# Kernel tuning notes

Hardware: AMD Instinct MI355X
Metric: run time of the kernel (lower is better)

## Reference

```python
import jax, jax.numpy as jnp
import numpy as np

N, B, D = 50000, 128, 35   # nodes, graphs, node_dim
T = 140                     # padded sequence length
EPS = 1e-5

def _gcn(x, W, b, src, dst):
    # PyG GCNConv: sym-normalized adjacency with self loops, then linear.
    h = x @ W
    deg = jnp.ones((N,), h.dtype).at[dst].add(1.0)  # in-degree + self loop
    dinv = jax.lax.rsqrt(deg)
    msg = h[src] * (dinv[src] * dinv[dst])[:, None]
    agg = jax.ops.segment_sum(msg, dst, num_segments=N)
    return agg + h * (dinv * dinv)[:, None] + b  # + self-loop messages + bias

def _bn(x, g, b):
    m = x.mean(0)
    v = x.var(0)
    return (x - m) * jax.lax.rsqrt(v + EPS) * g + b

def _lstm(xs, Wih, Whh, bih, bhh, reverse):
    # xs: [T, B, D]; torch LSTM gate order i,f,g,o; hidden size D
    def step(carry, xt):
        h, c = carry
        gates = xt @ Wih.T + h @ Whh.T + bih + bhh
        i, f, g, o = jnp.split(gates, 4, axis=-1)
        c = jax.nn.sigmoid(f) * c + jax.nn.sigmoid(i) * jnp.tanh(g)
        h = jax.nn.sigmoid(o) * jnp.tanh(c)
        return (h, c), h
    h0 = jnp.zeros((xs.shape[1], D), xs.dtype)
    _, hs = jax.lax.scan(step, (h0, h0), xs, reverse=reverse)
    return hs

def setup_inputs() -> dict:
    key = jax.random.key(0)
    ks = iter(jax.random.split(key, 64))
    def w(shape, s=0.05):
        return jax.random.normal(next(ks), shape, jnp.float32) * s
    inp = {
        'x': jax.random.normal(next(ks), (N, D), jnp.float32),
        'edge_intra': jax.random.randint(next(ks), (2, 300000), 0, N, jnp.int32),
        'edge_inter': jax.random.randint(next(ks), (2, 100000), 0, N, jnp.int32),
        'split': jax.random.randint(next(ks), (N,), 0, 2, jnp.int32),
        'batch': jnp.sort(jax.random.randint(next(ks), (N,), 0, B, jnp.int32)),
    }
    dims = [(35, 128), (128, 256), (256, 512), (512, 256), (256, 35)]
    for i, (di, do) in enumerate(dims, 1):
        inp[f'W{i}'] = w((di, do)); inp[f'b{i}'] = jnp.zeros((do,), jnp.float32)
        inp[f'g{i}'] = jnp.ones((do,), jnp.float32); inp[f'be{i}'] = jnp.zeros((do,), jnp.float32)
    for d in ('f', 'b'):  # bidirectional LSTM, 4*D = 140 gate rows
        inp[f'Wih_{d}'] = w((4 * D, D)); inp[f'Whh_{d}'] = w((4 * D, D))
        inp[f'bih_{d}'] = jnp.zeros((4 * D,), jnp.float32); inp[f'bhh_{d}'] = jnp.zeros((4 * D,), jnp.float32)
    for nm in ('q', 'k', 'v'):  # attention over d=2*D=70
        inp[f'W{nm}'] = w((2 * D, 2 * D)); inp[f'b{nm}'] = jnp.zeros((2 * D,), jnp.float32)
    inp['Wfc1'] = w((9800, 4340), 0.01); inp['bfc1'] = jnp.zeros((4340,), jnp.float32)
    inp['Wfc2'] = w((4340, 1), 0.01); inp['bfc2'] = jnp.zeros((1,), jnp.float32)
    return inp

def reference(x, edge_intra, edge_inter, split, batch,
              W1, b1, g1, be1, W2, b2, g2, be2, W3, b3, g3, be3,
              W4, b4, g4, be4, W5, b5, g5, be5,
              Wih_f, Whh_f, bih_f, bhh_f, Wih_b, Whh_b, bih_b, bhh_b,
              Wq, bq, Wk, bk, Wv, bv, Wfc1, bfc1, Wfc2, bfc2):
    src = jnp.concatenate([edge_intra[0], edge_inter[0]])
    dst = jnp.concatenate([edge_intra[1], edge_inter[1]])
    # conv1-3: relu then bn; conv4: bn then relu; conv5: bn only
    h = _bn(jax.nn.relu(_gcn(x, W1, b1, src, dst)), g1, be1)
    h = _bn(jax.nn.relu(_gcn(h, W2, b2, src, dst)), g2, be2)
    h = _bn(jax.nn.relu(_gcn(h, W3, b3, src, dst)), g3, be3)
    h = jax.nn.relu(_bn(_gcn(h, W4, b4, src, dst), g4, be4))
    h = _bn(_gcn(h, W5, b5, src, dst), g5, be5)
    # masked global_add_pool per split (avoids dynamic boolean indexing)
    is_pro = (split == 1).astype(h.dtype)[:, None]
    pro = jax.ops.segment_sum(h * is_pro, batch, num_segments=B)
    lig = jax.ops.segment_sum(h * (1.0 - is_pro), batch, num_segments=B)
    seq = jnp.concatenate([lig, pro], axis=1).reshape(B, 2, D)  # L = 2
    seq = jnp.pad(seq, ((0, 0), (0, T - 2), (0, 0)))            # [B,140,35]
    # attention mask, L=2 (static)
    m = jnp.eye(T, dtype=jnp.float32)
    m = m.at[2:, :].set(0.0).at[:, 2:].set(0.0)
    m = m.at[:, 1].set(1.0).at[1, :].set(1.0).at[1, 1].set(0.0)
    # BiLSTM over time axis
    xs = seq.transpose(1, 0, 2)  # [T,B,35]
    hf = _lstm(xs, Wih_f, Whh_f, bih_f, bhh_f, False)
    hb = _lstm(xs, Wih_b, Whh_b, bih_b, bhh_b, True)
    out = jnp.concatenate([hf, hb], axis=-1).transpose(1, 0, 2)  # [B,140,70]
    # masked single-head attention
    q = out @ Wq + bq
    k = out @ Wk + bk
    v = out @ Wv + bv
    sc = jnp.einsum('bqd,bkd->bqk', q, k) / jnp.sqrt(jnp.asarray(2.0 * D, out.dtype))
    sc = jnp.where(m[None] == 0, -1e9, sc)
    o = jax.nn.softmax(sc, axis=-1) @ v  # [B,140,70]
    f = jax.nn.relu(o.reshape(B, -1) @ Wfc1 + bfc1)
    return (f @ Wfc2 + bfc2).reshape(-1)
```

## Files before the change

### kernel.cpp

```cpp
#include <hip/hip_runtime.h>

#define N_NODES 50000
#define DIM0 35
#define BGRAPH 128
#define TSEQ 140
#define EPSBN 1e-5f
#define E_TOTAL 400000
#define E_INTRA 300000
#define E_INTER 100000
#define FC1_OUT 4340

typedef __attribute__((ext_vector_type(8))) short s8v;
typedef __attribute__((ext_vector_type(4))) short s4v;
typedef __attribute__((ext_vector_type(4))) float f32x4;

static __device__ __forceinline__ unsigned short bf16_rne(float x) {
    unsigned int u = __float_as_uint(x);
    unsigned int r = (u + 0x7FFFu + ((u >> 16) & 1u)) >> 16;
    return (unsigned short)r;
}
static __device__ __forceinline__ void bf16_split(float x, unsigned short& h, unsigned short& l) {
    h = bf16_rne(x);
    float hf = __uint_as_float(((unsigned int)h) << 16);
    l = bf16_rne(x - hf);
}

static __device__ __forceinline__ void edge_sd(int e, const int* intra, const int* inter, int& s, int& d) {
    if (e < E_INTRA) { s = intra[e]; d = intra[E_INTRA + e]; }
    else { int k = e - E_INTRA; s = inter[k]; d = inter[E_INTER + k]; }
}

__global__ void k_init(int* cnt, int* cursor, float* out, const float* bfc2, float* bnsumAll) {
    int i = blockIdx.x * 256 + threadIdx.x;
    if (i < N_NODES) { cnt[i] = 0; cursor[i] = 0; }
    if (i < BGRAPH) out[i] = bfc2[0];
    if (i < 5 * 1024) bnsumAll[i] = 0.f;
}

__global__ void k_deg(const int* intra, const int* inter, int* cnt) {
    int e = blockIdx.x * 256 + threadIdx.x;
    if (e >= E_TOTAL) return;
    int s, d; edge_sd(e, intra, inter, s, d);
    atomicAdd(&cnt[d], 1);
}

__global__ void k_scan1(const int* __restrict__ cnt, int* __restrict__ partial, int* __restrict__ blocksum,
                        float* __restrict__ dinv) {
    __shared__ int buf[256];
    int t = threadIdx.x;
    int i = blockIdx.x * 256 + t;
    int v = (i < N_NODES) ? cnt[i] : 0;
    if (i < N_NODES) dinv[i] = rsqrtf(1.0f + (float)v);
    buf[t] = v;
    __syncthreads();
    for (int off = 1; off < 256; off <<= 1) {
        int add = (t >= off) ? buf[t - off] : 0;
        __syncthreads();
        buf[t] += add;
        __syncthreads();
    }
    if (i < N_NODES) partial[i] = buf[t];
    if (t == 255) blocksum[blockIdx.x] = buf[255];
}

__global__ void k_scan2(int* blocksum, int nb) {
    __shared__ int buf[256];
    int t = threadIdx.x;
    buf[t] = (t < nb) ? blocksum[t] : 0;
    __syncthreads();
    for (int off = 1; off < 256; off <<= 1) {
        int add = (t >= off) ? buf[t - off] : 0;
        __syncthreads();
        buf[t] += add;
        __syncthreads();
    }
    if (t < nb) blocksum[t] = buf[t];
}

__global__ void k_scan3(const int* __restrict__ partial, const int* __restrict__ blocksum, int* __restrict__ rowptr) {
    int b = blockIdx.x;
    int i = b * 256 + threadIdx.x;
    if (i == 0) rowptr[0] = 0;
    if (i < N_NODES) {
        int off = (b == 0) ? 0 : blocksum[b - 1];
        rowptr[i + 1] = partial[i] + off;
    }
}

__global__ void k_scatter(const int* intra, const int* inter, const int* rowptr,
                          int* cursor, const float* dinv, int* srcs, float* coef) {
    int e = blockIdx.x * 256 + threadIdx.x;
    if (e >= E_TOTAL) return;
    int s, d; edge_sd(e, intra, inter, s, d);
    int p = rowptr[d] + atomicAdd(&cursor[d], 1);
    srcs[p] = s;
    coef[p] = dinv[s] * dinv[d];
}

__global__ __launch_bounds__(256) void k_agg_small(const float* __restrict__ X, float* __restrict__ Z,
        const int* __restrict__ rowptr, const int* __restrict__ srcs, const float* __restrict__ coef,
        const float* __restrict__ dinv, const float* __restrict__ bias) {
    int wave = threadIdx.x >> 6, lane = threadIdx.x & 63;
    int i = blockIdx.x * 4 + wave;
    if (i >= N_NODES || lane >= DIM0) return;
    int b0 = rowptr[i], e1 = rowptr[i + 1];
    float self = dinv[i] * dinv[i];
    float acc = X[(size_t)i * DIM0 + lane] * self;
    if (bias) acc += bias[lane];
    for (int k = b0; k < e1; ++k) acc += coef[k] * X[(size_t)srcs[k] * DIM0 + lane];
    Z[(size_t)i * DIM0 + lane] = acc;
}

__global__ __launch_bounds__(256) void k_agg_vec(const float* __restrict__ X, float* __restrict__ Z,
        const int* __restrict__ rowptr, const int* __restrict__ srcs, const float* __restrict__ coef,
        const float* __restrict__ dinv, const float* __restrict__ alpha, const float* __restrict__ beta,
        const float* __restrict__ bias, int d, int lpshift) {
    int i = (blockIdx.x * 256 + threadIdx.x) >> lpshift;
    int lane_in = threadIdx.x & ((1 << lpshift) - 1);
    if (i >= N_NODES) return;
    int b0 = rowptr[i], e1 = rowptr[i + 1];
    float self = dinv[i] * dinv[i];
    int c = lane_in * 4;
    float4 al, be;
    if (alpha) { al = *(const float4*)&alpha[c]; be = *(const float4*)&beta[c]; }
    else { al = make_float4(1.f, 1.f, 1.f, 1.f); be = make_float4(0.f, 0.f, 0.f, 0.f); }
    float4 xi = *(const float4*)&X[(size_t)i * d + c];
    float4 acc;
    acc.x = self * (al.x * xi.x + be.x);
    acc.y = self * (al.y * xi.y + be.y);
    acc.z = self * (al.z * xi.z + be.z);
    acc.w = self * (al.w * xi.w + be.w);
    if (bias) {
        float4 bi = *(const float4*)&bias[c];
        acc.x += bi.x; acc.y += bi.y; acc.z += bi.z; acc.w += bi.w;
    }
    for (int k = b0; k < e1; ++k) {
        int s = srcs[k];
        float cf = coef[k];
        float4 xs = *(const float4*)&X[(size_t)s * d + c];
        acc.x += cf * (al.x * xs.x + be.x);
        acc.y += cf * (al.y * xs.y + be.y);
        acc.z += cf * (al.z * xs.z + be.z);
        acc.w += cf * (al.w * xs.w + be.w);
    }
    *(float4*)&Z[(size_t)i * d + c] = acc;
}

__global__ __launch_bounds__(256) void k_gemm(const float* __restrict__ A, const float* __restrict__ W,
                                              const float* __restrict__ bias, float* __restrict__ C,
                                              int Mrows, int K, int Ncols, int relu,
                                              const float* __restrict__ alphaA, const float* __restrict__ betaA,
                                              int reluA) {
    __shared__ float As[64][17];
    __shared__ float Ws[16][65];
    int tid = threadIdx.x;
    int tx = tid & 15, ty = tid >> 4;
    int row0 = blockIdx.x * 64, col0 = blockIdx.y * 64;
    float acc[4][4] = {};
    for (int k0 = 0; k0 < K; k0 += 16) {
        for (int l = tid; l < 1024; l += 256) {
            int m = l >> 4, kk = l & 15;
            int r = row0 + m, k = k0 + kk;
            float v = 0.f;
            if (r < Mrows && k < K) {
                v = A[(size_t)r * K + k];
                if (alphaA) {
                    v = alphaA[k] * v + betaA[k];
                    if (reluA) v = fmaxf(v, 0.f);
                }
            }
            As[m][kk] = v;
        }
        for (int l = tid; l < 1024; l += 256) {
            int kk = l >> 6, n = l & 63;
            int k = k0 + kk, c = col0 + n;
            Ws[kk][n] = (k < K && c < Ncols) ? W[(size_t)k * Ncols + c] : 0.f;
        }
        __syncthreads();
#pragma unroll
        for (int kk = 0; kk < 16; ++kk) {
            float a[4], w[4];
#pragma unroll
            for (int i2 = 0; i2 < 4; ++i2) a[i2] = As[ty * 4 + i2][kk];
#pragma unroll
            for (int j = 0; j < 4; ++j) w[j] = Ws[kk][tx * 4 + j];
#pragma unroll
            for (int i2 = 0; i2 < 4; ++i2)
#pragma unroll
                for (int j = 0; j < 4; ++j)
                    acc[i2][j] += a[i2] * w[j];
        }
        __syncthreads();
    }
    for (int i2 = 0; i2 < 4; ++i2) {
        int r = row0 + ty * 4 + i2;
        if (r >= Mrows) continue;
        for (int j = 0; j < 4; ++j) {
            int c = col0 + tx * 4 + j;
            if (c >= Ncols) continue;
            float v = acc[i2][j];
            if (bias) v += bias[c];
            if (relu) v = fmaxf(v, 0.f);
            C[(size_t)r * Ncols + c] = v;
        }
    }
}

__global__ void k_wprep(const float* __restrict__ W, unsigned short* __restrict__ Wf, int K, int Ncols) {
    int gid = blockIdx.x * 256 + threadIdx.x;
    int KT = K >> 5;
    int total = (Ncols >> 4) * KT * 64;
    if (gid >= total) return;
    int lane = gid & 63;
    int f = gid >> 6;
    int kt = f % KT, ntile = f / KT;
    int n = ntile * 16 + (lane & 15);
    int kb = kt * 32 + (lane >> 4) * 8;
    size_t base = (size_t)f * 1024 + lane * 8;
#pragma unroll
    for (int j = 0; j < 8; ++j) {
        unsigned short h, l;
        bf16_split(W[(size_t)(kb + j) * Ncols + n], h, l);
        Wf[base + j] = h;
        Wf[base + 512 + j] = l;
    }
}

__global__ __launch_bounds__(256) void k_gemm_mfma(
    const float* __restrict__ A, const unsigned short* __restrict__ Wf,
    const float* __restrict__ bias, float* __restrict__ C,
    int Mrows, int K, int Ncols, int relu,
    const float* __restrict__ alphaA, const float* __restrict__ betaA,
    float* __restrict__ bnsum) {
    __shared__ unsigned short As[2][2][128][40];
    int tid = threadIdx.x;
    int lane = tid & 63, wave = tid >> 6;
    int wm = wave >> 1, wn = wave & 1;
    int row0 = blockIdx.x * 128;
    int nt0 = blockIdx.y * 8;
    int KT = K >> 5;

    f32x4 acc[4][4];
#pragma unroll
    for (int a = 0; a < 4; ++a)
#pragma unroll
        for (int b = 0; b < 4; ++b) acc[a][b] = (f32x4)0.f;

    float4 reg[4];
    auto load_chunk = [&](int kt) {
#pragma unroll
        for (int l = 0; l < 4; ++l) {
            int i = tid + l * 256;
            int m = i >> 3, kv = (i & 7) * 4;
            int r = row0 + m;
            float4 v = make_float4(0.f, 0.f, 0.f, 0.f);
            if (r < Mrows) v = *(const float4*)&A[(size_t)r * K + kt * 32 + kv];
            reg[l] = v;
        }
    };
    auto store_chunk = [&](int buf, int kt) {
#pragma unroll
        for (int l = 0; l < 4; ++l) {
            int i = tid + l * 256;
            int m = i >> 3, kv = (i & 7) * 4;
            float4 v = reg[l];
            if (alphaA) {
                int kg = kt * 32 + kv;
                float4 al = *(const float4*)&alphaA[kg];
                float4 be = *(const float4*)&betaA[kg];
                v.x = al.x * v.x + be.x;
                v.y = al.y * v.y + be.y;
                v.z = al.z * v.z + be.z;
                v.w = al.w * v.w + be.w;
            }
            unsigned short h0, l0, h1, l1, h2, l2, h3, l3;
            bf16_split(v.x, h0, l0); bf16_split(v.y, h1, l1);
            bf16_split(v.z, h2, l2); bf16_split(v.w, h3, l3);
            s4v hv = {(short)h0, (short)h1, (short)h2, (short)h3};
            s4v lv = {(short)l0, (short)l1, (short)l2, (short)l3};
            *(s4v*)&As[buf][0][m][kv] = hv;
            *(s4v*)&As[buf][1][m][kv] = lv;
        }
    };

    load_chunk(0);
    store_chunk(0, 0);
    __syncthreads();

    int mrow = wm * 64 + (lane & 15);
    int koff = (lane >> 4) * 8;

    for (int kt = 0; kt < KT; ++kt) {
        int cur = kt & 1;
        if (kt + 1 < KT) load_chunk(kt + 1);
        s8v bh[4], bl[4];
#pragma unroll
        for (int nt = 0; nt < 4; ++nt) {
            int ntg = nt0 + wn * 4 + nt;
            size_t fb = ((size_t)(ntg * KT + kt)) * 1024 + lane * 8;
            bh[nt] = *(const s8v*)&Wf[fb];
            bl[nt] = *(const s8v*)&Wf[fb + 512];
        }
        s8v ah[4], alo[4];
#pragma unroll
        for (int mt = 0; mt < 4; ++mt) {
            ah[mt]  = *(const s8v*)&As[cur][0][mrow + mt * 16][koff];
            alo[mt] = *(const s8v*)&As[cur][1][mrow + mt * 16][koff];
        }
#pragma unroll
        for (int nt = 0; nt < 4; ++nt)
#pragma unroll
            for (int mt = 0; mt < 4; ++mt) {
                acc[mt][nt] = __builtin_amdgcn_mfma_f32_16x16x32_bf16(ah[mt], bh[nt], acc[mt][nt], 0, 0, 0);
                acc[mt][nt] = __builtin_amdgcn_mfma_f32_16x16x32_bf16(ah[mt], bl[nt], acc[mt][nt], 0, 0, 0);
                acc[mt][nt] = __builtin_amdgcn_mfma_f32_16x16x32_bf16(alo[mt], bh[nt], acc[mt][nt], 0, 0, 0);
            }
        if (kt + 1 < KT) store_chunk(cur ^ 1, kt + 1);
        __syncthreads();
    }

#pragma unroll
    for (int nt = 0; nt < 4; ++nt) {
        int cg = (nt0 + wn * 4 + nt) * 16 + (lane & 15);
        float bia = bias ? bias[cg] : 0.f;
        float s1 = 0.f, s2 = 0.f;
#pragma unroll
        for (int mt = 0; mt < 4; ++mt) {
            int rbase = row0 + wm * 64 + mt * 16 + (lane >> 4) * 4;
#pragma unroll
            for (int r = 0; r < 4; ++r) {
                int rg = rbase + r;
                if (rg < Mrows) {
                    float v = acc[mt][nt][r] + bia;
                    if (relu) v = fmaxf(v, 0.f);
                    C[(size_t)rg * Ncols + cg] = v;
                    s1 += v; s2 += v * v;
                }
            }
        }
        if (bnsum) {
            s1 += __shfl_xor(s1, 16, 64);
            s1 += __shfl_xor(s1, 32, 64);
            s2 += __shfl_xor(s2, 16, 64);
            s2 += __shfl_xor(s2, 32, 64);
            if (lane < 16) {
                atomicAdd(&bnsum[cg], s1);
                atomicAdd(&bnsum[Ncols + cg], s2);
            }
        }
    }
}

__global__ void k_bn_stats(const float* __restrict__ X, float* sums, int d) {
    long long total = (long long)N_NODES * d;
    int G = gridDim.x * blockDim.x;
    int gid = blockIdx.x * blockDim.x + threadIdx.x;
    int c = gid % d;
    float s1 = 0.f, s2 = 0.f;
    for (long long i = gid; i < total; i += G) {
        float v = X[i];
        s1 += v; s2 += v * v;
    }
    atomicAdd(&sums[c], s1);
    atomicAdd(&sums[d + c], s2);
}

__global__ void k_bn_final(const float* sums, const float* g, const float* be,
                           float* alpha, float* beta, int d) {
    int c = threadIdx.x;
    if (c >= d) return;
    float mean = sums[c] / (float)N_NODES;
    float var = sums[d + c] / (float)N_NODES - mean * mean;
    float a = g[c] * rsqrtf(var + EPSBN);
    alpha[c] = a;
    beta[c] = be[c] - mean * a;
}

__global__ void k_pool(const float* __restrict__ h, const int* __restrict__ split,
                       const int* __restrict__ batch, float* lig, float* pro,
                       const float* __restrict__ alpha, const float* __restrict__ beta) {
    int b = blockIdx.x;
    __shared__ float sl[DIM0], sp[DIM0];
    __shared__ int s_start, s_end;
    if (threadIdx.x < DIM0) { sl[threadIdx.x] = 0.f; sp[threadIdx.x] = 0.f; }
    if (threadIdx.x == 0) {
        int lo = 0, hi = N_NODES;
        while (lo < hi) { int mid = (lo + hi) >> 1; if (batch[mid] < b) lo = mid + 1; else hi = mid; }
        s_start = lo;
        hi = N_NODES;
        while (lo < hi) { int mid = (lo + hi) >> 1; if (batch[mid] < b + 1) lo = mid + 1; else hi = mid; }
        s_end = lo;
    }
    __syncthreads();
    int start = s_start, end = s_end;
    for (int k = threadIdx.x; k < (end - start) * DIM0; k += blockDim.x) {
        int node = start + k / DIM0;
        int c = k % DIM0;
        float v = alpha[c] * h[(size_t)node * DIM0 + c] + beta[c];
        if (split[node] == 1) atomicAdd(&sp[c], v);
        else atomicAdd(&sl[c], v);
    }
    __syncthreads();
    if (threadIdx.x < DIM0) {
        lig[b * DIM0 + threadIdx.x] = sl[threadIdx.x];
        pro[b * DIM0 + threadIdx.x] = sp[threadIdx.x];
    }
}

__global__ __launch_bounds__(192) void k_lstm(
    const float* __restrict__ lig, const float* __restrict__ pro,
    const float* __restrict__ Wih_f, const float* __restrict__ Whh_f,
    const float* __restrict__ bih_f, const float* __restrict__ bhh_f,
    const float* __restrict__ Wih_b, const float* __restrict__ Whh_b,
    const float* __restrict__ bih_b, const float* __restrict__ bhh_b,
    float* __restrict__ outb) {
    int blk = blockIdx.x;
    int dir = blk >> 7;
    int b = blk & 127;
    const float* Wih = dir ? Wih_b : Wih_f;
    const float* Whh = dir ? Whh_b : Whh_f;
    const float* bih = dir ? bih_b : bih_f;
    const float* bhh = dir ? bhh_b : bhh_f;

    __shared__ float h_lds[DIM0];
    __shared__ float x_lds[2][DIM0];
    __shared__ float gate_lds[4 * DIM0];
    int t = threadIdx.x;
    float wih[DIM0], whh[DIM0], bsum = 0.f;
    if (t < 4 * DIM0) {
#pragma unroll
        for (int j = 0; j < DIM0; ++j) { wih[j] = Wih[t * DIM0 + j]; whh[j] = Whh[t * DIM0 + j]; }
        bsum = bih[t] + bhh[t];
    }
    if (t < DIM0) {
        x_lds[0][t] = lig[b * DIM0 + t];
        x_lds[1][t] = pro[b * DIM0 + t];
        h_lds[t] = 0.f;
    }
    float c_reg = 0.f;
    __syncthreads();
    for (int step = 0; step < TSEQ; ++step) {
        int tt = dir ? (TSEQ - 1 - step) : step;
        if (t < 4 * DIM0) {
            float acc = bsum;
            if (tt < 2) {
#pragma unroll
                for (int j = 0; j < DIM0; ++j) acc += wih[j] * x_lds[tt][j];
            }
#pragma unroll
            for (int j = 0; j < DIM0; ++j) acc += whh[j] * h_lds[j];
            gate_lds[t] = acc;
        }
        __syncthreads();
        if (t < DIM0) {
            float gi = gate_lds[t], gf = gate_lds[DIM0 + t];
            float gg = gate_lds[2 * DIM0 + t], go = gate_lds[3 * DIM0 + t];
            float si = 1.f / (1.f + expf(-gi));
            float sf = 1.f / (1.f + expf(-gf));
            float so = 1.f / (1.f + expf(-go));
            c_reg = sf * c_reg + si * tanhf(gg);
            float hv = so * tanhf(c_reg);
            h_lds[t] = hv;
            outb[((size_t)b * TSEQ + tt) * 70 + dir * DIM0 + t] = hv;
        }
        __syncthreads();
    }
}

__global__ void k_concatW(const float* __restrict__ Wq, const float* __restrict__ bq,
                          const float* __restrict__ Wk, const float* __restrict__ bk,
                          const float* __restrict__ Wv, const float* __restrict__ bv,
                          float* __restrict__ Wcat, float* __restrict__ bcat) {
    int idx = blockIdx.x * 256 + threadIdx.x;
    if (idx < 70 * 210) {
        int k = idx / 210, col = idx % 210;
        int g = col / 70, j = col % 70;
        const float* Wsrc = (g == 0) ? Wq : ((g == 1) ? Wk : Wv);
        Wcat[idx] = Wsrc[k * 70 + j];
    }
    if (idx < 210) {
        int g = idx / 70, j = idx % 70;
        const float* bsrc = (g == 0) ? bq : ((g == 1) ? bk : bv);
        bcat[idx] = bsrc[j];
    }
}

__global__ void k_attention(const float* __restrict__ qkv, float* __restrict__ osm) {
    int b = blockIdx.x;
    __shared__ float q0[70], q1[70], s[TSEQ];
    __shared__ float s00_s, s01_s, ssum_s;
    int t = threadIdx.x;
    const float* base = qkv + (size_t)b * TSEQ * 210;
    if (t < 70) {
        q0[t] = base[0 * 210 + t];
        q1[t] = base[1 * 210 + t];
    }
    __syncthreads();
    const float scale = rsqrtf(70.f);
    if (t < TSEQ) {
        const float* krow = base + (size_t)t * 210 + 70;
        float acc = 0.f;
        for (int j = 0; j < 70; ++j) acc += q1[j] * krow[j];
        s[t] = acc * scale;
    } else if (t == TSEQ || t == TSEQ + 1) {
        int kk = t - TSEQ;
        const float* krow = base + (size_t)kk * 210 + 70;
        float acc = 0.f;
        for (int j = 0; j < 70; ++j) acc += q0[j] * krow[j];
        if (kk) s01_s = acc * scale; else s00_s = acc * scale;
    }
    __syncthreads();
    if (t == 0) {
        float mx = -1e30f;
        for (int i = 0; i < TSEQ; ++i) if (i != 1) mx = fmaxf(mx, s[i]);
        float sum = 0.f;
        for (int i = 0; i < TSEQ; ++i) {
            float e = (i == 1) ? 0.f : expf(s[i] - mx);
            s[i] = e; sum += e;
        }
        ssum_s = sum;
    }
    __syncthreads();
    if (t < 70) {
        float inv = 1.f / ssum_s;
        float acc = 0.f;
        for (int i = 0; i < TSEQ; ++i) acc += s[i] * base[(size_t)i * 210 + 140 + t];
        float o1v = acc * inv;
        float m0 = fmaxf(s00_s, s01_s);
        float e0 = expf(s00_s - m0), e1 = expf(s01_s - m0);
        float w0 = e0 / (e0 + e1), w1 = e1 / (e0 + e1);
        float v0 = base[0 * 210 + 140 + t];
        float v1 = base[1 * 210 + 140 + t];
        osm[b * 210 + t] = w0 * v0 + w1 * v1;
        osm[b * 210 + 70 + t] = o1v;
        osm[b * 210 + 140 + t] = v1;
    }
}

__global__ void k_wsum(const float* __restrict__ Wfc1, float* __restrict__ Wsum) {
    int idx = blockIdx.x * 256 + threadIdx.x;
    if (idx >= 70 * FC1_OUT) return;
    int j = idx / FC1_OUT, c = idx % FC1_OUT;
    float acc = 0.f;
    for (int tt = 2; tt < TSEQ; ++tt) acc += Wfc1[((size_t)(tt * 70 + j)) * FC1_OUT + c];
    Wsum[(size_t)j * FC1_OUT + c] = acc;
}

__global__ __launch_bounds__(256) void k_fc(const float* __restrict__ osm, const float* __restrict__ Wfc1,
                                            const float* __restrict__ Wsum, const float* __restrict__ bfc1,
                                            const float* __restrict__ Wfc2, float* __restrict__ out) {
    __shared__ float olds[8][210];
    __shared__ float wred[4][8];
    int g = blockIdx.y;
    int c = blockIdx.x * 256 + threadIdx.x;
    for (int l = threadIdx.x; l < 8 * 210; l += 256)
        olds[l / 210][l % 210] = osm[(g * 8 + l / 210) * 210 + (l % 210)];
    __syncthreads();
    float acc[8] = {};
    if (c < FC1_OUT) {
        for (int j = 0; j < 140; ++j) {
            float w = Wfc1[(size_t)j * FC1_OUT + c];
#pragma unroll
            for (int b = 0; b < 8; ++b) acc[b] = fmaf(olds[b][j], w, acc[b]);
        }
        for (int j = 0; j < 70; ++j) {
            float w = Wsum[(size_t)j * FC1_OUT + c];
#pragma unroll
            for (int b = 0; b < 8; ++b) acc[b] = fmaf(olds[b][140 + j], w, acc[b]);
        }
        float bb = bfc1[c], pw = Wfc2[c];
#pragma unroll
        for (int b = 0; b < 8; ++b) acc[b] = fmaxf(acc[b] + bb, 0.f) * pw;
    }
#pragma unroll
    for (int b = 0; b < 8; ++b) {
        acc[b] += __shfl_down(acc[b], 32, 64);
        acc[b] += __shfl_down(acc[b], 16, 64);
        acc[b] += __shfl_down(acc[b], 8, 64);
        acc[b] += __shfl_down(acc[b], 4, 64);
        acc[b] += __shfl_down(acc[b], 2, 64);
        acc[b] += __shfl_down(acc[b], 1, 64);
    }
    int wave = threadIdx.x >> 6;
    if ((threadIdx.x & 63) == 0)
#pragma unroll
        for (int b = 0; b < 8; ++b) wred[wave][b] = acc[b];
    __syncthreads();
    if (threadIdx.x < 8) {
        float t = wred[0][threadIdx.x] + wred[1][threadIdx.x] + wred[2][threadIdx.x] + wred[3][threadIdx.x];
        atomicAdd(&out[g * 8 + threadIdx.x], t);
    }
}

extern "C" void kernel_launch(void* const* d_in, const int* in_sizes, int n_in,
                              void* d_out, int out_size, void* d_ws, size_t ws_size,
                              hipStream_t stream) {
    const float* x = (const float*)d_in[0];
    const int* intra = (const int*)d_in[1];
    const int* inter = (const int*)d_in[2];
    const int* split = (const int*)d_in[3];
    const int* batch = (const int*)d_in[4];
    const float *W[5], *bW[5], *gW[5], *beW[5];
    for (int i = 0; i < 5; ++i) {
        W[i]   = (const float*)d_in[5 + 4 * i];
        bW[i]  = (const float*)d_in[6 + 4 * i];
        gW[i]  = (const float*)d_in[7 + 4 * i];
        beW[i] = (const float*)d_in[8 + 4 * i];
    }
    const float* Wih_f = (const float*)d_in[25];
    const float* Whh_f = (const float*)d_in[26];
    const float* bih_f = (const float*)d_in[27];
    const float* bhh_f = (const float*)d_in[28];
    const float* Wih_b = (const float*)d_in[29];
    const float* Whh_b = (const float*)d_in[30];
    const float* bih_b = (const float*)d_in[31];
    const float* bhh_b = (const float*)d_in[32];
    const float* Wq = (const float*)d_in[33];
    const float* bq = (const float*)d_in[34];
    const float* Wk = (const float*)d_in[35];
    const float* bk = (const float*)d_in[36];
    const float* Wv = (const float*)d_in[37];
    const float* bv = (const float*)d_in[38];
    const float* Wfc1 = (const float*)d_in[39];
    const float* bfc1 = (const float*)d_in[40];
    const float* Wfc2 = (const float*)d_in[41];
    const float* bfc2 = (const float*)d_in[42];

    char* p = (char*)d_ws;
    auto carve = [&](size_t bytes) {
        char* r = p;
        p += (bytes + 255) & ~(size_t)255;
        return r;
    };
    float* bufA = (float*)carve((size_t)N_NODES * 512 * 4);
    float* bufB = (float*)carve((size_t)N_NODES * 256 * 4);
    float* bufM = (float*)carve((size_t)N_NODES * 256 * 4);
    float* dinv = (float*)carve((size_t)N_NODES * 4);
    int* cnt    = (int*)carve((size_t)N_NODES * 4);
    int* rowptr = (int*)carve((size_t)(N_NODES + 1) * 4);
    int* cursor = (int*)carve((size_t)N_NODES * 4);
    int* scanp  = (int*)carve((size_t)N_NODES * 4);
    int* bsums  = (int*)carve(256 * 4);
    int* srcs   = (int*)carve((size_t)E_TOTAL * 4);
    float* coef = (float*)carve((size_t)E_TOTAL * 4);
    float* bnsumAll = (float*)carve(5 * 1024 * 4);
    float* alphaAll = (float*)carve(5 * 512 * 4);
    float* betaAll  = (float*)carve(5 * 512 * 4);
    float* lig = (float*)carve((size_t)BGRAPH * DIM0 * 4);
    float* pro = (float*)carve((size_t)BGRAPH * DIM0 * 4);
    float* outb = (float*)carve((size_t)BGRAPH * TSEQ * 70 * 4);
    float* qkvb = (float*)carve((size_t)BGRAPH * TSEQ * 210 * 4);
    float* Wcat = (float*)carve((size_t)70 * 210 * 4);
    float* bcat = (float*)carve(210 * 4);
    float* osm = (float*)carve((size_t)BGRAPH * 210 * 4);
    float* wsum = (float*)carve((size_t)70 * FC1_OUT * 4);
    unsigned short* Wf2 = (unsigned short*)carve((size_t)128 * 256 * 2 * 2);
    unsigned short* Wf3 = (unsigned short*)carve((size_t)256 * 512 * 2 * 2);
    unsigned short* Wf4 = (unsigned short*)carve((size_t)512 * 256 * 2 * 2);

    float* out = (float*)d_out;

    const int SCAN_B = (N_NODES + 255) / 256;

    k_init<<<(N_NODES + 255) / 256, 256, 0, stream>>>(cnt, cursor, out, bfc2, bnsumAll);
    k_deg<<<(E_TOTAL + 255) / 256, 256, 0, stream>>>(intra, inter, cnt);
    k_scan1<<<SCAN_B, 256, 0, stream>>>(cnt, scanp, bsums, dinv);
    k_scan2<<<1, 256, 0, stream>>>(bsums, SCAN_B);
    k_scan3<<<SCAN_B, 256, 0, stream>>>(scanp, bsums, rowptr);
    k_scatter<<<(E_TOTAL + 255) / 256, 256, 0, stream>>>(intra, inter, rowptr, cursor, dinv, srcs, coef);
    k_concatW<<<(70 * 210 + 255) / 256, 256, 0, stream>>>(Wq, bq, Wk, bk, Wv, bv, Wcat, bcat);
    k_wprep<<<((256 / 16) * (128 / 32) * 64 + 255) / 256, 256, 0, stream>>>(W[1], Wf2, 128, 256);
    k_wprep<<<((512 / 16) * (256 / 32) * 64 + 255) / 256, 256, 0, stream>>>(W[2], Wf3, 256, 512);
    k_wprep<<<((256 / 16) * (512 / 32) * 64 + 255) / 256, 256, 0, stream>>>(W[3], Wf4, 512, 256);

    auto BN = [&](int layer) { return bnsumAll + layer * 1024; };
    auto AL = [&](int layer) { return alphaAll + layer * 512; };
    auto BE = [&](int layer) { return betaAll + layer * 512; };
    auto bn_final = [&](int layer, int d) {
        k_bn_final<<<1, 512, 0, stream>>>(BN(layer), gW[layer], beW[layer], AL(layer), BE(layer), d);
    };

    const int GB64 = (N_NODES + 63) / 64;
    const int GB128 = (N_NODES + 127) / 128;
    const int AGG4 = (N_NODES + 3) / 4;
    const int AGG8 = (N_NODES + 7) / 8;

    k_agg_small<<<AGG4, 256, 0, stream>>>(x, bufM, rowptr, srcs, coef, dinv, nullptr);
    k_gemm<<<dim3(GB64, 2), 256, 0, stream>>>(bufM, W[0], bW[0], bufA, N_NODES, 35, 128, 1, nullptr, nullptr, 0);
    k_bn_stats<<<128, 256, 0, stream>>>(bufA, BN(0), 128);
    bn_final(0, 128);
    k_agg_vec<<<AGG8, 256, 0, stream>>>(bufA, bufM, rowptr, srcs, coef, dinv, AL(0), BE(0), nullptr, 128, 5);
    k_gemm_mfma<<<dim3(GB128, 2), 256, 0, stream>>>(bufM, Wf2, bW[1], bufB, N_NODES, 128, 256, 1, nullptr, nullptr, BN(1));
    bn_final(1, 256);
    k_agg_vec<<<AGG4, 256, 0, stream>>>(bufB, bufM, rowptr, srcs, coef, dinv, AL(1), BE(1), nullptr, 256, 6);
    k_gemm_mfma<<<dim3(GB128, 4), 256, 0, stream>>>(bufM, Wf3, bW[2], bufA, N_NODES, 256, 512, 1, nullptr, nullptr, BN(2));
    bn_final(2, 512);
    k_gemm_mfma<<<dim3(GB128, 2), 256, 0, stream>>>(bufA, Wf4, nullptr, bufM, N_NODES, 512, 256, 0, AL(2), BE(2), nullptr);
    k_agg_vec<<<AGG4, 256, 0, stream>>>(bufM, bufB, rowptr, srcs, coef, dinv, nullptr, nullptr, bW[3], 256, 6);
    k_bn_stats<<<256, 256, 0, stream>>>(bufB, BN(3), 256);
    bn_final(3, 256);
    k_gemm<<<dim3(GB64, 1), 256, 0, stream>>>(bufB, W[4], nullptr, bufM, N_NODES, 256, 35, 0, AL(3), BE(3), 1);
    k_agg_small<<<AGG4, 256, 0, stream>>>(bufM, bufA, rowptr, srcs, coef, dinv, bW[4]);
    k_bn_stats<<<35, 256, 0, stream>>>(bufA, BN(4), 35);
    bn_final(4, 35);

    k_pool<<<BGRAPH, 256, 0, stream>>>(bufA, split, batch, lig, pro, AL(4), BE(4));

    k_lstm<<<256, 192, 0, stream>>>(lig, pro, Wih_f, Whh_f, bih_f, bhh_f,
                                    Wih_b, Whh_b, bih_b, bhh_b, outb);

    k_gemm<<<dim3((BGRAPH * TSEQ + 63) / 64, 4), 256, 0, stream>>>(outb, Wcat, bcat, qkvb,
                                                                   BGRAPH * TSEQ, 70, 210, 0, nullptr, nullptr, 0);

    k_attention<<<BGRAPH, 256, 0, stream>>>(qkvb, osm);

    k_wsum<<<(70 * FC1_OUT + 255) / 256, 256, 0, stream>>>(Wfc1, wsum);
    k_fc<<<dim3(17, 16), 256, 0, stream>>>(osm, Wfc1, wsum, bfc1, Wfc2, out);
}
```

Measured before the change: 1.087 ms.

## Pre-split GEMM activations into bf16 hi/lo in producers and fold BN into weights

The aggregation and GEMM epilogues now write activations directly as separate bf16 hi and lo arrays, so the MFMA GEMM loads bf16 tiles straight into LDS and no longer converts fp32 per tile. For layer 4 the BatchNorm affine is folded into the weight prep (row scale) plus a precomputed bias vector instead of being applied to activations. Buffers are reorganized and aliased. This cuts the fp32 A-operand traffic and the per-block split work, at the cost of the layer-3 GEMM writing two bf16 outputs and a small serial bias kernel.

Result: slower. 1.198 ms (+10.2%).

```diff
diff --git a/kernel.cpp b/kernel.cpp
--- a/kernel.cpp
+++ b/kernel.cpp
@@ -113,27 +113,48 @@
 
 __global__ __launch_bounds__(256) void k_agg_vec(const float* __restrict__ X, float* __restrict__ Z,
         const int* __restrict__ rowptr, const int* __restrict__ srcs, const float* __restrict__ coef,
-        const float* __restrict__ dinv, const float* __restrict__ alpha, const float* __restrict__ beta,
-        const float* __restrict__ bias, int d, int lpshift) {
+        const float* __restrict__ dinv, const float* __restrict__ bias, int d, int lpshift) {
     int i = (blockIdx.x * 256 + threadIdx.x) >> lpshift;
     int lane_in = threadIdx.x & ((1 << lpshift) - 1);
     if (i >= N_NODES) return;
     int b0 = rowptr[i], e1 = rowptr[i + 1];
     float self = dinv[i] * dinv[i];
     int c = lane_in * 4;
-    float4 al, be;
-    if (alpha) { al = *(const float4*)&alpha[c]; be = *(const float4*)&beta[c]; }
-    else { al = make_float4(1.f, 1.f, 1.f, 1.f); be = make_float4(0.f, 0.f, 0.f, 0.f); }
+    float4 xi = *(const float4*)&X[(size_t)i * d + c];
+    float4 acc;
+    acc.x = self * xi.x; acc.y = self * xi.y; acc.z = self * xi.z; acc.w = self * xi.w;
+    if (bias) {
+        float4 bi = *(const float4*)&bias[c];
+        acc.x += bi.x; acc.y += bi.y; acc.z += bi.z; acc.w += bi.w;
+    }
+    for (int k = b0; k < e1; ++k) {
+        int s = srcs[k];
+        float cf = coef[k];
+        float4 xs = *(const float4*)&X[(size_t)s * d + c];
+        acc.x += cf * xs.x; acc.y += cf * xs.y; acc.z += cf * xs.z; acc.w += cf * xs.w;
+    }
+    *(float4*)&Z[(size_t)i * d + c] = acc;
+}
+
+__global__ __launch_bounds__(256) void k_agg_split(const float* __restrict__ X,
+        unsigned short* __restrict__ Ahi, unsigned short* __restrict__ Alo,
+        const int* __restrict__ rowptr, const int* __restrict__ srcs, const float* __restrict__ coef,
+        const float* __restrict__ dinv, const float* __restrict__ alpha, const float* __restrict__ beta,
+        int d, int lpshift) {
+    int i = (blockIdx.x * 256 + threadIdx.x) >> lpshift;
+    int lane_in = threadIdx.x & ((1 << lpshift) - 1);
+    if (i >= N_NODES) return;
+    int b0 = rowptr[i], e1 = rowptr[i + 1];
+    float self = dinv[i] * dinv[i];
+    int c = lane_in * 4;
+    float4 al = *(const float4*)&alpha[c];
+    float4 be = *(const float4*)&beta[c];
     float4 xi = *(const float4*)&X[(size_t)i * d + c];
     float4 acc;
     acc.x = self * (al.x * xi.x + be.x);
     acc.y = self * (al.y * xi.y + be.y);
     acc.z = self * (al.z * xi.z + be.z);
     acc.w = self * (al.w * xi.w + be.w);
-    if (bias) {
-        float4 bi = *(const float4*)&bias[c];
-        acc.x += bi.x; acc.y += bi.y; acc.z += bi.z; acc.w += bi.w;
-    }
     for (int k = b0; k < e1; ++k) {
         int s = srcs[k];
         float cf = coef[k];
@@ -143,7 +164,13 @@
         acc.z += cf * (al.z * xs.z + be.z);
         acc.w += cf * (al.w * xs.w + be.w);
     }
-    *(float4*)&Z[(size_t)i * d + c] = acc;
+    unsigned short h0, l0, h1, l1, h2, l2, h3, l3;
+    bf16_split(acc.x, h0, l0); bf16_split(acc.y, h1, l1);
+    bf16_split(acc.z, h2, l2); bf16_split(acc.w, h3, l3);
+    s4v hv = {(short)h0, (short)h1, (short)h2, (short)h3};
+    s4v lv = {(short)l0, (short)l1, (short)l2, (short)l3};
+    *(s4v*)&Ahi[(size_t)i * d + c] = hv;
+    *(s4v*)&Alo[(size_t)i * d + c] = lv;
 }
 
 __global__ __launch_bounds__(256) void k_gemm(const float* __restrict__ A, const float* __restrict__ W,
@@ -206,7 +233,8 @@
     }
 }
 
-__global__ void k_wprep(const float* __restrict__ W, unsigned short* __restrict__ Wf, int K, int Ncols) {
+__global__ void k_wprep(const float* __restrict__ W, unsigned short* __restrict__ Wf, int K, int Ncols,
+                        const float* __restrict__ rowscale) {
     int gid = blockIdx.x * 256 + threadIdx.x;
     int KT = K >> 5;
     int total = (Ncols >> 4) * KT * 64;
@@ -219,19 +247,29 @@
     size_t base = (size_t)f * 1024 + lane * 8;
 #pragma unroll
     for (int j = 0; j < 8; ++j) {
+        float v = W[(size_t)(kb + j) * Ncols + n];
+        if (rowscale) v *= rowscale[kb + j];
         unsigned short h, l;
-        bf16_split(W[(size_t)(kb + j) * Ncols + n], h, l);
+        bf16_split(v, h, l);
         Wf[base + j] = h;
         Wf[base + 512 + j] = l;
     }
 }
 
-__global__ __launch_bounds__(256) void k_gemm_mfma(
-    const float* __restrict__ A, const unsigned short* __restrict__ Wf,
-    const float* __restrict__ bias, float* __restrict__ C,
-    int Mrows, int K, int Ncols, int relu,
-    const float* __restrict__ alphaA, const float* __restrict__ betaA,
-    float* __restrict__ bnsum) {
+__global__ void k_bnbias(const float* __restrict__ W, const float* __restrict__ beta,
+                         float* __restrict__ bv, int K, int Ncols) {
+    int c = blockIdx.x * 256 + threadIdx.x;
+    if (c >= Ncols) return;
+    float acc = 0.f;
+    for (int k = 0; k < K; ++k) acc += beta[k] * W[(size_t)k * Ncols + c];
+    bv[c] = acc;
+}
+
+__global__ __launch_bounds__(256) void k_gemm_mfma2(
+    const unsigned short* __restrict__ Ahi, const unsigned short* __restrict__ Alo,
+    const unsigned short* __restrict__ Wf, const float* __restrict__ bias,
+    float* __restrict__ C, unsigned short* __restrict__ Chi, unsigned short* __restrict__ Clo,
+    int Mrows, int K, int Ncols, int relu, float* __restrict__ bnsum) {
     __shared__ unsigned short As[2][2][128][40];
     int tid = threadIdx.x;
     int lane = tid & 63, wave = tid >> 6;
@@ -246,53 +284,42 @@
 #pragma unroll
         for (int b = 0; b < 4; ++b) acc[a][b] = (f32x4)0.f;
 
-    float4 reg[4];
-    auto load_chunk = [&](int kt) {
-#pragma unroll
-        for (int l = 0; l < 4; ++l) {
-            int i = tid + l * 256;
-            int m = i >> 3, kv = (i & 7) * 4;
+    s8v rh[2], rl[2];
+    auto stage_regs = [&](int kt) {
+#pragma unroll
+        for (int l = 0; l < 2; ++l) {
+            int j = tid + l * 256;
+            int m = j >> 2, ko = (j & 3) * 8;
             int r = row0 + m;
-            float4 v = make_float4(0.f, 0.f, 0.f, 0.f);
-            if (r < Mrows) v = *(const float4*)&A[(size_t)r * K + kt * 32 + kv];
-            reg[l] = v;
+            s8v h = (s8v)0, lo = (s8v)0;
+            if (r < Mrows) {
+                size_t off = (size_t)r * K + kt * 32 + ko;
+                h = *(const s8v*)&Ahi[off];
+                lo = *(const s8v*)&Alo[off];
+            }
+            rh[l] = h; rl[l] = lo;
         }
     };
-    auto store_chunk = [&](int buf, int kt) {
-#pragma unroll
-        for (int l = 0; l < 4; ++l) {
-            int i = tid + l * 256;
-            int m = i >> 3, kv = (i & 7) * 4;
-            float4 v = reg[l];
-            if (alphaA) {
-                int kg = kt * 32 + kv;
-                float4 al = *(const float4*)&alphaA[kg];
-                float4 be = *(const float4*)&betaA[kg];
-                v.x = al.x * v.x + be.x;
-                v.y = al.y * v.y + be.y;
-                v.z = al.z * v.z + be.z;
-                v.w = al.w * v.w + be.w;
-            }
-            unsigned short h0, l0, h1, l1, h2, l2, h3, l3;
-            bf16_split(v.x, h0, l0); bf16_split(v.y, h1, l1);
-            bf16_split(v.z, h2, l2); bf16_split(v.w, h3, l3);
-            s4v hv = {(short)h0, (short)h1, (short)h2, (short)h3};
-            s4v lv = {(short)l0, (short)l1, (short)l2, (short)l3};
-            *(s4v*)&As[buf][0][m][kv] = hv;
-            *(s4v*)&As[buf][1][m][kv] = lv;
+    auto write_lds = [&](int buf) {
+#pragma unroll
+        for (int l = 0; l < 2; ++l) {
+            int j = tid + l * 256;
+            int m = j >> 2, ko = (j & 3) * 8;
+            *(s8v*)&As[buf][0][m][ko] = rh[l];
+            *(s8v*)&As[buf][1][m][ko] = rl[l];
         }
     };
 
-    load_chunk(0);
-    store_chunk(0, 0);
+    stage_regs(0);
+    write_lds(0);
     __syncthreads();
 
     int mrow = wm * 64 + (lane & 15);
     int koff = (lane >> 4) * 8;
+    int cur = 0;
 
     for (int kt = 0; kt < KT; ++kt) {
-        int cur = kt & 1;
-        if (kt + 1 < KT) load_chunk(kt + 1);
+        if (kt + 1 < KT) stage_regs(kt + 1);
         s8v bh[4], bl[4];
 #pragma unroll
         for (int nt = 0; nt < 4; ++nt) {
@@ -315,8 +342,9 @@
                 acc[mt][nt] = __builtin_amdgcn_mfma_f32_16x16x32_bf16(ah[mt], bl[nt], acc[mt][nt], 0, 0, 0);
                 acc[mt][nt] = __builtin_amdgcn_mfma_f32_16x16x32_bf16(alo[mt], bh[nt], acc[mt][nt], 0, 0, 0);
             }
-        if (kt + 1 < KT) store_chunk(cur ^ 1, kt + 1);
-        __syncthreads();
+        if (kt + 1 < KT) write_lds(cur ^ 1);
+        __syncthreads();
+        cur ^= 1;
     }
 
 #pragma unroll
@@ -333,7 +361,13 @@
                 if (rg < Mrows) {
                     float v = acc[mt][nt][r] + bia;
                     if (relu) v = fmaxf(v, 0.f);
-                    C[(size_t)rg * Ncols + cg] = v;
+                    if (C) C[(size_t)rg * Ncols + cg] = v;
+                    if (Chi) {
+                        unsigned short h, l;
+                        bf16_split(v, h, l);
+                        Chi[(size_t)rg * Ncols + cg] = h;
+                        Clo[(size_t)rg * Ncols + cg] = l;
+                    }
                     s1 += v; s2 += v * v;
                 }
             }
@@ -632,7 +666,13 @@
         p += (bytes + 255) & ~(size_t)255;
         return r;
     };
-    float* bufA = (float*)carve((size_t)N_NODES * 512 * 4);
+    unsigned short* A2hi = (unsigned short*)carve((size_t)N_NODES * 128 * 2);
+    unsigned short* A2lo = (unsigned short*)carve((size_t)N_NODES * 128 * 2);
+    unsigned short* A3hi = (unsigned short*)carve((size_t)N_NODES * 256 * 2);
+    unsigned short* A3lo = (unsigned short*)carve((size_t)N_NODES * 256 * 2);
+    unsigned short* A4hi = (unsigned short*)carve((size_t)N_NODES * 512 * 2);
+    unsigned short* A4lo = (unsigned short*)carve((size_t)N_NODES * 512 * 2);
+    float* bufA = (float*)carve((size_t)N_NODES * 128 * 4);
     float* bufB = (float*)carve((size_t)N_NODES * 256 * 4);
     float* bufM = (float*)carve((size_t)N_NODES * 256 * 4);
     float* dinv = (float*)carve((size_t)N_NODES * 4);
@@ -646,17 +686,18 @@
     float* bnsumAll = (float*)carve(5 * 1024 * 4);
     float* alphaAll = (float*)carve(5 * 512 * 4);
     float* betaAll  = (float*)carve(5 * 512 * 4);
+    float* bv4  = (float*)carve(256 * 4);
     float* lig = (float*)carve((size_t)BGRAPH * DIM0 * 4);
     float* pro = (float*)carve((size_t)BGRAPH * DIM0 * 4);
-    float* outb = (float*)carve((size_t)BGRAPH * TSEQ * 70 * 4);
-    float* qkvb = (float*)carve((size_t)BGRAPH * TSEQ * 210 * 4);
     float* Wcat = (float*)carve((size_t)70 * 210 * 4);
     float* bcat = (float*)carve(210 * 4);
     float* osm = (float*)carve((size_t)BGRAPH * 210 * 4);
-    float* wsum = (float*)carve((size_t)70 * FC1_OUT * 4);
     unsigned short* Wf2 = (unsigned short*)carve((size_t)128 * 256 * 2 * 2);
     unsigned short* Wf3 = (unsigned short*)carve((size_t)256 * 512 * 2 * 2);
     unsigned short* Wf4 = (unsigned short*)carve((size_t)512 * 256 * 2 * 2);
+    float* outb = (float*)A2hi;
+    float* qkvb = outb + (size_t)BGRAPH * TSEQ * 70;
+    float* wsum = qkvb + (size_t)BGRAPH * TSEQ * 210;
 
     float* out = (float*)d_out;
 
@@ -669,9 +710,8 @@
     k_scan3<<<SCAN_B, 256, 0, stream>>>(scanp, bsums, rowptr);
     k_scatter<<<(E_TOTAL + 255) / 256, 256, 0, stream>>>(intra, inter, rowptr, cursor, dinv, srcs, coef);
     k_concatW<<<(70 * 210 + 255) / 256, 256, 0, stream>>>(Wq, bq, Wk, bk, Wv, bv, Wcat, bcat);
-    k_wprep<<<((256 / 16) * (128 / 32) * 64 + 255) / 256, 256, 0, stream>>>(W[1], Wf2, 128, 256);
-    k_wprep<<<((512 / 16) * (256 / 32) * 64 + 255) / 256, 256, 0, stream>>>(W[2], Wf3, 256, 512);
-    k_wprep<<<((256 / 16) * (512 / 32) * 64 + 255) / 256, 256, 0, stream>>>(W[3], Wf4, 512, 256);
+    k_wprep<<<((256 / 16) * (128 / 32) * 64 + 255) / 256, 256, 0, stream>>>(W[1], Wf2, 128, 256, nullptr);
+    k_wprep<<<((512 / 16) * (256 / 32) * 64 + 255) / 256, 256, 0, stream>>>(W[2], Wf3, 256, 512, nullptr);
 
     auto BN = [&](int layer) { return bnsumAll + layer * 1024; };
     auto AL = [&](int layer) { return alphaAll + layer * 512; };
@@ -689,14 +729,19 @@
     k_gemm<<<dim3(GB64, 2), 256, 0, stream>>>(bufM, W[0], bW[0], bufA, N_NODES, 35, 128, 1, nullptr, nullptr, 0);
     k_bn_stats<<<128, 256, 0, stream>>>(bufA, BN(0), 128);
     bn_final(0, 128);
-    k_agg_vec<<<AGG8, 256, 0, stream>>>(bufA, bufM, rowptr, srcs, coef, dinv, AL(0), BE(0), nullptr, 128, 5);
-    k_gemm_mfma<<<dim3(GB128, 2), 256, 0, stream>>>(bufM, Wf2, bW[1], bufB, N_NODES, 128, 256, 1, nullptr, nullptr, BN(1));
+    k_agg_split<<<AGG8, 256, 0, stream>>>(bufA, A2hi, A2lo, rowptr, srcs, coef, dinv, AL(0), BE(0), 128, 5);
+    k_gemm_mfma2<<<dim3(GB128, 2), 256, 0, stream>>>(A2hi, A2lo, Wf2, bW[1], bufB, nullptr, nullptr,
+                                                     N_NODES, 128, 256, 1, BN(1));
     bn_final(1, 256);
-    k_agg_vec<<<AGG4, 256, 0, stream>>>(bufB, bufM, rowptr, srcs, coef, dinv, AL(1), BE(1), nullptr, 256, 6);
-    k_gemm_mfma<<<dim3(GB128, 4), 256, 0, stream>>>(bufM, Wf3, bW[2], bufA, N_NODES, 256, 512, 1, nullptr, nullptr, BN(2));
+    k_agg_split<<<AGG4, 256, 0, stream>>>(bufB, A3hi, A3lo, rowptr, srcs, coef, dinv, AL(1), BE(1), 256, 6);
+    k_gemm_mfma2<<<dim3(GB128, 4), 256, 0, stream>>>(A3hi, A3lo, Wf3, bW[2], nullptr, A4hi, A4lo,
+                                                     N_NODES, 256, 512, 1, BN(2));
     bn_final(2, 512);
-    k_gemm_mfma<<<dim3(GB128, 2), 256, 0, stream>>>(bufA, Wf4, nullptr, bufM, N_NODES, 512, 256, 0, AL(2), BE(2), nullptr);
-    k_agg_vec<<<AGG4, 256, 0, stream>>>(bufM, bufB, rowptr, srcs, coef, dinv, nullptr, nullptr, bW[3], 256, 6);
+    k_wprep<<<((256 / 16) * (512 / 32) * 64 + 255) / 256, 256, 0, stream>>>(W[3], Wf4, 512, 256, AL(2));
+    k_bnbias<<<1, 256, 0, stream>>>(W[3], BE(2), bv4, 512, 256);
+    k_gemm_mfma2<<<dim3(GB128, 2), 256, 0, stream>>>(A4hi, A4lo, Wf4, bv4, bufM, nullptr, nullptr,
+                                                     N_NODES, 512, 256, 0, nullptr);
+    k_agg_vec<<<AGG4, 256, 0, stream>>>(bufM, bufB, rowptr, srcs, coef, dinv, bW[3], 256, 6);
     k_bn_stats<<<256, 256, 0, stream>>>(bufB, BN(3), 256);
     bn_final(3, 256);
     k_gemm<<<dim3(GB64, 1), 256, 0, stream>>>(bufB, W[4], nullptr, bufM, N_NODES, 256, 35, 0, AL(3), BE(3), 1);
```

## Fold BN affine into layer-4 weights and swap grid axes for row-tile locality

Applied to the files above, without the earlier changes.

The batch-norm scale of layer 3 is folded into the bf16-split weights of the layer-4 GEMM, and its shift becomes a precomputed bias vector accumulated by a new small kernel. This removes the per-element alpha/beta transform from the GEMM's A-load path. All GEMM launches also swap grid x/y so that column tiles of the same row block run next to each other, which should improve L2 reuse of A. The cost is an extra weight-prep pass and an atomic bias kernel sitting between the layer-3 GEMM and the layer-4 GEMM. Because the weights are scaled before the bf16 split, rounding changes slightly.

Measured after the change: 1.072 ms. No clear change (-1.4%).

```diff
diff --git a/kernel.cpp b/kernel.cpp
--- a/kernel.cpp
+++ b/kernel.cpp
@@ -30,11 +30,12 @@
     else { int k = e - E_INTRA; s = inter[k]; d = inter[E_INTER + k]; }
 }
 
-__global__ void k_init(int* cnt, int* cursor, float* out, const float* bfc2, float* bnsumAll) {
+__global__ void k_init(int* cnt, int* cursor, float* out, const float* bfc2, float* bnsumAll, float* bv4) {
     int i = blockIdx.x * 256 + threadIdx.x;
     if (i < N_NODES) { cnt[i] = 0; cursor[i] = 0; }
     if (i < BGRAPH) out[i] = bfc2[0];
     if (i < 5 * 1024) bnsumAll[i] = 0.f;
+    if (i < 256) bv4[i] = 0.f;
 }
 
 __global__ void k_deg(const int* intra, const int* inter, int* cnt) {
@@ -155,7 +156,7 @@
     __shared__ float Ws[16][65];
     int tid = threadIdx.x;
     int tx = tid & 15, ty = tid >> 4;
-    int row0 = blockIdx.x * 64, col0 = blockIdx.y * 64;
+    int row0 = blockIdx.y * 64, col0 = blockIdx.x * 64;
     float acc[4][4] = {};
     for (int k0 = 0; k0 < K; k0 += 16) {
         for (int l = tid; l < 1024; l += 256) {
@@ -206,7 +207,8 @@
     }
 }
 
-__global__ void k_wprep(const float* __restrict__ W, unsigned short* __restrict__ Wf, int K, int Ncols) {
+__global__ void k_wprep(const float* __restrict__ W, unsigned short* __restrict__ Wf, int K, int Ncols,
+                        const float* __restrict__ rowscale) {
     int gid = blockIdx.x * 256 + threadIdx.x;
     int KT = K >> 5;
     int total = (Ncols >> 4) * KT * 64;
@@ -219,11 +221,24 @@
     size_t base = (size_t)f * 1024 + lane * 8;
 #pragma unroll
     for (int j = 0; j < 8; ++j) {
+        float v = W[(size_t)(kb + j) * Ncols + n];
+        if (rowscale) v *= rowscale[kb + j];
         unsigned short h, l;
-        bf16_split(W[(size_t)(kb + j) * Ncols + n], h, l);
+        bf16_split(v, h, l);
         Wf[base + j] = h;
         Wf[base + 512 + j] = l;
     }
+}
+
+__global__ void k_bnbias(const float* __restrict__ W, const float* __restrict__ beta,
+                         float* __restrict__ bv, int K, int Ncols) {
+    int c = threadIdx.x;
+    if (c >= Ncols) return;
+    int k0 = blockIdx.x * 16;
+    float acc = 0.f;
+#pragma unroll
+    for (int k = 0; k < 16; ++k) acc += beta[k0 + k] * W[(size_t)(k0 + k) * Ncols + c];
+    atomicAdd(&bv[c], acc);
 }
 
 __global__ __launch_bounds__(256) void k_gemm_mfma(
@@ -236,8 +251,8 @@
     int tid = threadIdx.x;
     int lane = tid & 63, wave = tid >> 6;
     int wm = wave >> 1, wn = wave & 1;
-    int row0 = blockIdx.x * 128;
-    int nt0 = blockIdx.y * 8;
+    int row0 = blockIdx.y * 128;
+    int nt0 = blockIdx.x * 8;
     int KT = K >> 5;
 
     f32x4 acc[4][4];
@@ -646,6 +661,7 @@
     float* bnsumAll = (float*)carve(5 * 1024 * 4);
     float* alphaAll = (float*)carve(5 * 512 * 4);
     float* betaAll  = (float*)carve(5 * 512 * 4);
+    float* bv4  = (float*)carve(256 * 4);
     float* lig = (float*)carve((size_t)BGRAPH * DIM0 * 4);
     float* pro = (float*)carve((size_t)BGRAPH * DIM0 * 4);
     float* outb = (float*)carve((size_t)BGRAPH * TSEQ * 70 * 4);
@@ -662,16 +678,15 @@
 
     const int SCAN_B = (N_NODES + 255) / 256;
 
-    k_init<<<(N_NODES + 255) / 256, 256, 0, stream>>>(cnt, cursor, out, bfc2, bnsumAll);
+    k_init<<<(N_NODES + 255) / 256, 256, 0, stream>>>(cnt, cursor, out, bfc2, bnsumAll, bv4);
     k_deg<<<(E_TOTAL + 255) / 256, 256, 0, stream>>>(intra, inter, cnt);
     k_scan1<<<SCAN_B, 256, 0, stream>>>(cnt, scanp, bsums, dinv);
     k_scan2<<<1, 256, 0, stream>>>(bsums, SCAN_B);
     k_scan3<<<SCAN_B, 256, 0, stream>>>(scanp, bsums, rowptr);
     k_scatter<<<(E_TOTAL + 255) / 256, 256, 0, stream>>>(intra, inter, rowptr, cursor, dinv, srcs, coef);
     k_concatW<<<(70 * 210 + 255) / 256, 256, 0, stream>>>(Wq, bq, Wk, bk, Wv, bv, Wcat, bcat);
-    k_wprep<<<((256 / 16) * (128 / 32) * 64 + 255) / 256, 256, 0, stream>>>(W[1], Wf2, 128, 256);
-    k_wprep<<<((512 / 16) * (256 / 32) * 64 + 255) / 256, 256, 0, stream>>>(W[2], Wf3, 256, 512);
-    k_wprep<<<((256 / 16) * (512 / 32) * 64 + 255) / 256, 256, 0, stream>>>(W[3], Wf4, 512, 256);
+    k_wprep<<<((256 / 16) * (128 / 32) * 64 + 255) / 256, 256, 0, stream>>>(W[1], Wf2, 128, 256, nullptr);
+    k_wprep<<<((512 / 16) * (256 / 32) * 64 + 255) / 256, 256, 0, stream>>>(W[2], Wf3, 256, 512, nullptr);
 
     auto BN = [&](int layer) { return bnsumAll + layer * 1024; };
     auto AL = [&](int layer) { return alphaAll + layer * 512; };
@@ -686,20 +701,25 @@
     const int AGG8 = (N_NODES + 7) / 8;
 
     k_agg_small<<<AGG4, 256, 0, stream>>>(x, bufM, rowptr, srcs, coef, dinv, nullptr);
-    k_gemm<<<dim3(GB64, 2), 256, 0, stream>>>(bufM, W[0], bW[0], bufA, N_NODES, 35, 128, 1, nullptr, nullptr, 0);
+    k_gemm<<<dim3(2, GB64), 256, 0, stream>>>(bufM, W[0], bW[0], bufA, N_NODES, 35, 128, 1, nullptr, nullptr, 0);
     k_bn_stats<<<128, 256, 0, stream>>>(bufA, BN(0), 128);
     bn_final(0, 128);
     k_agg_vec<<<AGG8, 256, 0, stream>>>(bufA, bufM, rowptr, srcs, coef, dinv, AL(0), BE(0), nullptr, 128, 5);
-    k_gemm_mfma<<<dim3(GB128, 2), 256, 0, stream>>>(bufM, Wf2, bW[1], bufB, N_NODES, 128, 256, 1, nullptr, nullptr, BN(1));
+    k_gemm_mfma<<<dim3(2, GB128), 256, 0, stream>>>(bufM, Wf2, bW[1], bufB, N_NODES, 128, 256, 1,
+                                                    nullptr, nullptr, BN(1));
     bn_final(1, 256);
     k_agg_vec<<<AGG4, 256, 0, stream>>>(bufB, bufM, rowptr, srcs, coef, dinv, AL(1), BE(1), nullptr, 256, 6);
-    k_gemm_mfma<<<dim3(GB128, 4), 256, 0, stream>>>(bufM, Wf3, bW[2], bufA, N_NODES, 256, 512, 1, nullptr, nullptr, BN(2));
+    k_gemm_mfma<<<dim3(4, GB128), 256, 0, stream>>>(bufM, Wf3, bW[2], bufA, N_NODES, 256, 512, 1,
+                                                    nullptr, nullptr, BN(2));
     bn_final(2, 512);
-    k_gemm_mfma<<<dim3(GB128, 2), 256, 0, stream>>>(bufA, Wf4, nullptr, bufM, N_NODES, 512, 256, 0, AL(2), BE(2), nullptr);
+    k_wprep<<<((256 / 16) * (512 / 32) * 64 + 255) / 256, 256, 0, stream>>>(W[3], Wf4, 512, 256, AL(2));
+    k_bnbias<<<512 / 16, 256, 0, stream>>>(W[3], BE(2), bv4, 512, 256);
+    k_gemm_mfma<<<dim3(2, GB128), 256, 0, stream>>>(bufA, Wf4, bv4, bufM, N_NODES, 512, 256, 0,
+                                                    nullptr, nullptr, nullptr);
     k_agg_vec<<<AGG4, 256, 0, stream>>>(bufM, bufB, rowptr, srcs, coef, dinv, nullptr, nullptr, bW[3], 256, 6);
     k_bn_stats<<<256, 256, 0, stream>>>(bufB, BN(3), 256);
     bn_final(3, 256);
-    k_gemm<<<dim3(GB64, 1), 256, 0, stream>>>(bufB, W[4], nullptr, bufM, N_NODES, 256, 35, 0, AL(3), BE(3), 1);
+    k_gemm<<<dim3(1, GB64), 256, 0, stream>>>(bufB, W[4], nullptr, bufM, N_NODES, 256, 35, 0, AL(3), BE(3), 1);
     k_agg_small<<<AGG4, 256, 0, stream>>>(bufM, bufA, rowptr, srcs, coef, dinv, bW[4]);
     k_bn_stats<<<35, 256, 0, stream>>>(bufA, BN(4), 35);
     bn_final(4, 35);
@@ -709,7 +729,7 @@
     k_lstm<<<256, 192, 0, stream>>>(lig, pro, Wih_f, Whh_f, bih_f, bhh_f,
                                     Wih_b, Whh_b, bih_b, bhh_b, outb);
 
-    k_gemm<<<dim3((BGRAPH * TSEQ + 63) / 64, 4), 256, 0, stream>>>(outb, Wcat, bcat, qkvb,
+    k_gemm<<<dim3(4, (BGRAPH * TSEQ + 63) / 64), 256, 0, stream>>>(outb, Wcat, bcat, qkvb,
                                                                    BGRAPH * TSEQ, 70, 210, 0, nullptr, nullptr, 0);
 
     k_attention<<<BGRAPH, 256, 0, stream>>>(qkvb, osm);
```
